# Kernel tuning notes

Hardware: AMD Instinct MI355X
Metric: run time of the kernel (lower is better)

The kernel has to match this reference:

```python
import jax, jax.numpy as jnp
import numpy as np

B, N, D = 8, 8192, 512
H, WIDTH = 8, 2048
DH = D // H
EPS = 1e-5


def _ln(x, g, b):
    m = jnp.mean(x, axis=-1, keepdims=True)
    v = jnp.mean(jnp.square(x - m), axis=-1, keepdims=True)
    return (x - m) * jax.lax.rsqrt(v + EPS) * g + b


def setup_inputs() -> dict:
    key = jax.random.key(0)
    ks = jax.random.split(key, 16)
    s = 0.02
    return {
        "x": jax.random.normal(ks[0], (B, N, D), dtype=jnp.float32),
        "mask": jnp.ones((B, N), dtype=jnp.float32),
        "Wq": jax.random.normal(ks[1], (D, D), dtype=jnp.float32) * s,
        "bq": jnp.zeros((D,), dtype=jnp.float32),
        "Wk": jax.random.normal(ks[2], (D, D), dtype=jnp.float32) * s,
        "bk": jnp.zeros((D,), dtype=jnp.float32),
        "Wv": jax.random.normal(ks[3], (D, D), dtype=jnp.float32) * s,
        "bv": jnp.zeros((D,), dtype=jnp.float32),
        "q_alpha": jax.random.normal(ks[4], (H, DH), dtype=jnp.float32),
        "k_beta": jax.random.normal(ks[5], (H, DH), dtype=jnp.float32),
        "Wo": jax.random.normal(ks[6], (D, D), dtype=jnp.float32) * s,
        "bo": jnp.zeros((D,), dtype=jnp.float32),
        "ln0_g": jnp.ones((D,), dtype=jnp.float32),
        "ln0_b": jnp.zeros((D,), dtype=jnp.float32),
        "ln1_g": jnp.ones((D,), dtype=jnp.float32),
        "ln1_b": jnp.zeros((D,), dtype=jnp.float32),
        "W1": jax.random.normal(ks[7], (WIDTH, D), dtype=jnp.float32) * s,
        "b1": jnp.zeros((WIDTH,), dtype=jnp.float32),
        "W2": jax.random.normal(ks[8], (D, WIDTH), dtype=jnp.float32) * s,
        "b2": jnp.zeros((D,), dtype=jnp.float32),
    }


def reference(x, mask, Wq, bq, Wk, bk, Wv, bv, q_alpha, k_beta, Wo, bo,
              ln0_g, ln0_b, ln1_g, ln1_b, W1, b1, W2, b2):
    scale = DH ** -0.5
    mask_ = mask[..., None]                       # [B,N,1]
    valid = (mask != 0)[..., None]                # [B,N,1] bool, broadcast over H

    residual = x
    xn = _ln(x, ln0_g, ln0_b) * mask_

    Q = (xn @ Wq.T + bq).reshape(B, N, H, DH)
    K = (xn @ Wk.T + bk).reshape(B, N, H, DH)
    V = (xn @ Wv.T + bv).reshape(B, N, H, DH)

    # stage 1: global query pooling
    alpha = jnp.einsum('bnhd,hd->bnh', Q, q_alpha) * scale
    alpha = jnp.where(valid, alpha, -jnp.inf)
    alpha = jax.nn.softmax(alpha, axis=1)         # softmax over N
    global_q = jnp.einsum('bnhd,bnh->bhd', Q, alpha)

    # stage 2: global value pooling
    P = K * global_q[:, None]                     # [B,N,H,DH]
    beta = jnp.einsum('bnhd,hd->bnh', P, k_beta) * scale
    beta = jnp.where(valid, beta, -jnp.inf)
    beta = jax.nn.softmax(beta, axis=1)
    global_v = jnp.einsum('bnhd,bnh->bhd', V, beta)

    out = (Q + global_v[:, None]).reshape(B, N, D)
    out = out @ Wo.T + bo
    x = residual + out

    residual = x
    xn = _ln(x, ln1_g, ln1_b)
    h = jax.nn.gelu(xn @ W1.T + b1, approximate=False)
    h = jax.nn.gelu(h @ W2.T + b2, approximate=False)
    x = residual + h
    x = x * mask_
    return x
```

## Files before the change

kernel.cpp:

```cpp
#include <hip/hip_runtime.h>
#include <hip/hip_bf16.h>
#include <hip/hip_fp8.h>
#include <math.h>

typedef short s8v __attribute__((ext_vector_type(8)));
typedef short s4v __attribute__((ext_vector_type(4)));
typedef __bf16 bf8v __attribute__((ext_vector_type(8)));
typedef float f4v __attribute__((ext_vector_type(4)));
typedef long l2v __attribute__((ext_vector_type(2)));

#define GLOBAL_AS __attribute__((address_space(1)))
#define LDS_AS __attribute__((address_space(3)))

static __device__ __forceinline__ float bf2f(ushort u) {
  return __builtin_bit_cast(float, (unsigned int)u << 16);
}
static __device__ __forceinline__ ushort f2bf(float f) {
  unsigned int u = __builtin_bit_cast(unsigned int, f);
  u += 0x7FFFu + ((u >> 16) & 1u);
  return (ushort)(u >> 16);
}
static __device__ __forceinline__ unsigned char f2fp8(float f) {
#if __has_builtin(__builtin_amdgcn_cvt_pk_fp8_f32)
  int p = __builtin_amdgcn_cvt_pk_fp8_f32(f, f, 0, false);
  return (unsigned char)(p & 0xFF);
#else
  __hip_fp8_e4m3 v(f);
  return (unsigned char)v.__x;
#endif
}
static __device__ __forceinline__ float gelu_f(float v) {
  float t = v * v;
  float u = v * (0.0356774081f * t + 0.7978845608f);
  float e = __expf(-2.0f * u);
  return v * __builtin_amdgcn_rcpf(1.0f + e);
}
static __device__ __forceinline__ float wave_max_f(float v) {
  #pragma unroll
  for (int o = 32; o >= 1; o >>= 1) v = fmaxf(v, __shfl_xor(v, o));
  return v;
}
static __device__ __forceinline__ float wave_sum_f(float v) {
  #pragma unroll
  for (int o = 32; o >= 1; o >>= 1) v += __shfl_xor(v, o);
  return v;
}
static __device__ __forceinline__ void gload16(const void* g, const void* l) {
  __builtin_amdgcn_global_load_lds(
      (const GLOBAL_AS unsigned int*)g,
      (LDS_AS unsigned int*)l, 16, 0, 0);
}

__global__ void cvt_f32_fp8il(const float* __restrict__ in,
                              unsigned char* __restrict__ out, int n, int kmask) {
  int i = (blockIdx.x * 256 + threadIdx.x) * 4;
  if (i >= n) return;
  float4 v = *(const float4*)(in + i);
  const int k = i & kmask;
  const int r = k & 63;
  const int qq = (r >> 3) & 3, h = (r >> 5) & 1, j = r & 7;
  const long o = (long)(i - r) + qq * 16 + h * 8 + j;
  uchar4 ob;
  ob.x = f2fp8(v.x * 8.f); ob.y = f2fp8(v.y * 8.f);
  ob.z = f2fp8(v.z * 8.f); ob.w = f2fp8(v.w * 8.f);
  *(uchar4*)(out + o) = ob;
}

__global__ void cvt_w1_fp8il(const float* __restrict__ in,
                             unsigned char* __restrict__ out) {
  int i = (blockIdx.x * 256 + threadIdx.x) * 4;
  const int ro = i >> 9;
  const int k4 = i & 511;
  const int g = ro >> 6, fr = ro & 63;
  const int L = fr & 15, nn = fr >> 4;
  const int sr = g * 64 + ((L >> 1) & 1) * 32 + (L >> 2) * 8 + (L & 1) * 4 + nn;
  float4 v = *(const float4*)(in + (long)sr * 512 + k4);
  const int r = k4 & 63;
  const int o = (k4 - r) + ((r >> 3) & 3) * 16 + (r >> 5) * 8 + (r & 7);
  uchar4 ob;
  ob.x = f2fp8(v.x * 8.f); ob.y = f2fp8(v.y * 8.f);
  ob.z = f2fp8(v.z * 8.f); ob.w = f2fp8(v.w * 8.f);
  *(uchar4*)(out + (long)ro * 512 + o) = ob;
}

__global__ void perm_b1(const float* __restrict__ b1, float* __restrict__ b1p) {
  const int p = blockIdx.x * 256 + threadIdx.x;
  const int g = p >> 6, r = p & 63;
  const int kc = ((r >> 3) & 1) * 32 + (r >> 4) * 8 + ((r >> 2) & 1) * 4 + (r & 3);
  b1p[p] = b1[g * 64 + kc];
}

__global__ __launch_bounds__(256) void transpose512(
    const float* __restrict__ in, float* __restrict__ out) {
  __shared__ float t[32][33];
  const int bx = blockIdx.x & 15, by = blockIdx.x >> 4;
  const int tx = threadIdx.x & 31, ty = threadIdx.x >> 5;
  #pragma unroll
  for (int i = 0; i < 4; ++i)
    t[ty + i * 8][tx] = in[(long)(by * 32 + ty + i * 8) * 512 + bx * 32 + tx];
  __syncthreads();
  #pragma unroll
  for (int i = 0; i < 4; ++i)
    out[(long)(bx * 32 + ty + i * 8) * 512 + by * 32 + tx] = t[tx][ty + i * 8];
}

__global__ __launch_bounds__(256) void wqo_kernel(
    const float* __restrict__ Wo, const float* __restrict__ Wq,
    ushort* __restrict__ WqoB)
{
  __shared__ float lO[64][33];
  __shared__ float lQ[32][65];
  const int t = threadIdx.x;
  const int bi = (blockIdx.x & 7) * 64, bj = (blockIdx.x >> 3) * 64;
  float acc[16] = {};
  for (int k0 = 0; k0 < 512; k0 += 32) {
    __syncthreads();
    {
      const int r = t >> 2, c = (t & 3) * 8;
      #pragma unroll
      for (int j = 0; j < 8; ++j) lO[r][c + j] = Wo[(long)(bi + r) * 512 + k0 + c + j];
      const int r2 = t >> 3, c2 = (t & 7) * 8;
      #pragma unroll
      for (int j = 0; j < 8; ++j) lQ[r2][c2 + j] = Wq[(long)(k0 + r2) * 512 + bj + c2 + j];
    }
    __syncthreads();
    const int j = t & 63, ig = t >> 6;
    for (int kk = 0; kk < 32; ++kk) {
      float q = lQ[kk][j];
      #pragma unroll
      for (int ii = 0; ii < 16; ++ii) acc[ii] += lO[ig * 16 + ii][kk] * q;
    }
  }
  const int j = t & 63, ig = t >> 6;
  #pragma unroll
  for (int ii = 0; ii < 16; ++ii)
    WqoB[(long)(bi + ig * 16 + ii) * 512 + bj + j] = f2bf(acc[ii]);
}

__global__ __launch_bounds__(256) void wa_kernel(
    const float* __restrict__ qa, const float* __restrict__ Wq,
    const float* __restrict__ bqv, ushort* __restrict__ waB, float* __restrict__ ca)
{
  __shared__ float ql[64];
  const int h = blockIdx.x;
  const int t = threadIdx.x;
  if (h >= 8) {
    waB[h * 512 + t] = 0; waB[h * 512 + 256 + t] = 0;
    if (t == 0) ca[h] = 0.f;
    return;
  }
  if (t < 64) ql[t] = qa[h * 64 + t];
  __syncthreads();
  #pragma unroll
  for (int half = 0; half < 2; ++half) {
    const int k = half * 256 + t;
    float s = 0;
    for (int dd = 0; dd < 64; ++dd) s += ql[dd] * Wq[(long)(h * 64 + dd) * 512 + k];
    waB[h * 512 + k] = f2bf(s);
  }
  if (t == 0) {
    float s = 0;
    for (int dd = 0; dd < 64; ++dd) s += ql[dd] * bqv[h * 64 + dd];
    ca[h] = s;
  }
}

__global__ __launch_bounds__(256) void ln0_alpha(
    const float* __restrict__ x, const float* __restrict__ gam,
    const float* __restrict__ bet, const float* __restrict__ mask,
    const ushort* __restrict__ waB, const float* __restrict__ ca,
    ushort* __restrict__ out, float* __restrict__ AL)
{
  __shared__ ushort wal[8 * 512];
  const int tid = threadIdx.x, lane = tid & 63, wv = tid >> 6;
  *(s8v*)(wal + tid * 8) = *(const s8v*)(waB + tid * 8);
  *(s8v*)(wal + 2048 + tid * 8) = *(const s8v*)(waB + 2048 + tid * 8);
  const float* gp = gam + lane * 8;
  const float* bp = bet + lane * 8;
  float4 g0 = *(const float4*)gp, g1 = *(const float4*)(gp + 4);
  float4 c0 = *(const float4*)bp, c1 = *(const float4*)(bp + 4);
  const float gg[8] = {g0.x, g0.y, g0.z, g0.w, g1.x, g1.y, g1.z, g1.w};
  const float cc[8] = {c0.x, c0.y, c0.z, c0.w, c1.x, c1.y, c1.z, c1.w};
  __syncthreads();
  const long row0 = (long)blockIdx.x * 16 + wv * 4;
  for (int rr = 0; rr < 4; ++rr) {
    const long row = row0 + rr;
    const float* xp = x + row * 512 + lane * 8;
    float4 a = *(const float4*)xp;
    float4 b = *(const float4*)(xp + 4);
    float s = a.x + a.y + a.z + a.w + b.x + b.y + b.z + b.w;
    float q = a.x*a.x + a.y*a.y + a.z*a.z + a.w*a.w
            + b.x*b.x + b.y*b.y + b.z*b.z + b.w*b.w;
    s = wave_sum_f(s); q = wave_sum_f(q);
    const float m = s * (1.f / 512.f);
    const float var = q * (1.f / 512.f) - m * m;
    const float r = rsqrtf(var + 1e-5f);
    const float mk = mask[row];
    const float xin[8] = {a.x, a.y, a.z, a.w, b.x, b.y, b.z, b.w};
    float of[8];
    s8v o;
    #pragma unroll
    for (int j = 0; j < 8; ++j) {
      of[j] = ((xin[j] - m) * r * gg[j] + cc[j]) * mk;
      o[j] = (short)f2bf(of[j]);
    }
    *(s8v*)(out + row * 512 + lane * 8) = o;
    float dh[8];
    #pragma unroll
    for (int h = 0; h < 8; ++h) {
      s8v wa8 = *(const s8v*)(wal + h * 512 + lane * 8);
      float d = 0.f;
      #pragma unroll
      for (int j = 0; j < 8; ++j) d += of[j] * bf2f((ushort)wa8[j]);
      dh[h] = wave_sum_f(d);
    }
    if (lane == 0) {
      const int bb = (int)(row >> 13);
      const int n = (int)(row & 8191);
      #pragma unroll
      for (int h = 0; h < 8; ++h) {
        float lg = (dh[h] + ca[h]) * 0.125f;
        if (mk == 0.f) lg = -1e30f;
        AL[((long)((bb << 3) + h) << 13) + n] = lg;
      }
    }
  }
}

__global__ __launch_bounds__(256) void ln_rows_fp8il(
    const ushort* __restrict__ x, const float* __restrict__ gam,
    const float* __restrict__ bet, unsigned char* __restrict__ out)
{
  const int tid = threadIdx.x, lane = tid & 63, wv = tid >> 6;
  const long row = (long)blockIdx.x * 4 + wv;
  s8v v = *(const s8v*)(x + row * 512 + lane * 8);
  float xv[8];
  #pragma unroll
  for (int j = 0; j < 8; ++j) xv[j] = bf2f((ushort)v[j]);
  float s = 0.f, q = 0.f;
  #pragma unroll
  for (int j = 0; j < 8; ++j) { s += xv[j]; q += xv[j] * xv[j]; }
  s = wave_sum_f(s); q = wave_sum_f(q);
  float m = s * (1.f / 512.f);
  float var = q * (1.f / 512.f) - m * m;
  float r = rsqrtf(var + 1e-5f);
  const float* gp = gam + lane * 8;
  const float* bp = bet + lane * 8;
  float4 g0 = *(const float4*)gp, g1 = *(const float4*)(gp + 4);
  float4 c0 = *(const float4*)bp, c1 = *(const float4*)(bp + 4);
  float gg[8] = {g0.x, g0.y, g0.z, g0.w, g1.x, g1.y, g1.z, g1.w};
  float cc[8] = {c0.x, c0.y, c0.z, c0.w, c1.x, c1.y, c1.z, c1.w};
  unsigned long long pk = 0;
  #pragma unroll
  for (int j = 0; j < 8; ++j) {
    unsigned char b8 = f2fp8((xv[j] - m) * r * gg[j] + cc[j]);
    pk |= (unsigned long long)b8 << (8 * j);
  }
  *(unsigned long long*)(out + row * 512 + (lane >> 3) * 64
                         + (lane & 3) * 16 + ((lane >> 2) & 1) * 8) = pk;
}

template<int BS, int CS>
__global__ __launch_bounds__(256) void logits_k(
    const ushort* __restrict__ XN, const ushort* __restrict__ Wl,
    const float* __restrict__ cvec, const float* __restrict__ mask,
    float* __restrict__ outL)
{
  __shared__ ushort lw[16 * 512];
  __shared__ __align__(16) ushort lx[64 * 512];
  const int tid = threadIdx.x, lane = tid & 63, wv = tid >> 6;
  const long r0 = (long)blockIdx.x * 64;
  const int b = (int)(r0 >> 13);
  #pragma unroll
  for (int i = 0; i < 16; ++i) {
    const int U = i * 256 + tid;
    const int r = U >> 6, u1 = U & 63;
    const int us = u1 ^ (r & 7);
    gload16(XN + (r0 + r) * 512 + us * 8, lx + (long)U * 8);
  }
  #pragma unroll
  for (int i = 0; i < 4; ++i) {
    const int u = tid + i * 256;
    const int h2 = u >> 6, uu = u & 63;
    s8v v = *(const s8v*)(Wl + (long)b * BS + h2 * 512 + uu * 8);
    *(s8v*)(lw + h2 * 512 + (uu ^ (h2 & 7)) * 8) = v;
  }
  __syncthreads();
  const int h = lane & 15, q = lane >> 4;
  const int rloc = wv * 16 + (lane & 15);
  const ushort* axp = lx + rloc * 512;
  f4v acc = {};
  #pragma unroll
  for (int t = 0; t < 16; ++t) {
    bf8v a = *(const bf8v*)(axp + (((t * 4 + q) ^ (rloc & 7))) * 8);
    bf8v bb = *(const bf8v*)(lw + h * 512 + (((t * 4 + q) ^ (h & 7))) * 8);
    acc = __builtin_amdgcn_mfma_f32_16x16x32_bf16(a, bb, acc, 0, 0, 0);
  }
  const float cv = cvec[b * CS + h];
  const long rw = r0 + wv * 16;
  #pragma unroll
  for (int j = 0; j < 4; ++j) {
    const long n = rw + q * 4 + j;
    float v = (acc[j] + cv) * 0.125f;
    if (mask[n] == 0.f) v = -1e30f;
    if (h < 8) outL[((long)((b << 3) + h) << 13) + (n & 8191)] = v;
  }
}

__global__ __launch_bounds__(1024) void softmax_rows(float* __restrict__ L)
{
  __shared__ float red[16];
  __shared__ float bc;
  const int tid = threadIdx.x, lane = tid & 63, wv = tid >> 6;
  float* p = L + ((long)blockIdx.x << 13) + tid * 8;
  float4 v0 = *(float4*)p;
  float4 v1 = *(float4*)(p + 4);
  float m = fmaxf(fmaxf(fmaxf(v0.x, v0.y), fmaxf(v0.z, v0.w)),
                  fmaxf(fmaxf(v1.x, v1.y), fmaxf(v1.z, v1.w)));
  m = wave_max_f(m);
  if (lane == 0) red[wv] = m;
  __syncthreads();
  if (tid < 64) {
    float t = (lane < 16) ? red[lane] : -INFINITY;
    t = wave_max_f(t);
    if (lane == 0) bc = t;
  }
  __syncthreads();
  const float gm = bc;
  v0.x = __expf(v0.x - gm); v0.y = __expf(v0.y - gm);
  v0.z = __expf(v0.z - gm); v0.w = __expf(v0.w - gm);
  v1.x = __expf(v1.x - gm); v1.y = __expf(v1.y - gm);
  v1.z = __expf(v1.z - gm); v1.w = __expf(v1.w - gm);
  float s = v0.x + v0.y + v0.z + v0.w + v1.x + v1.y + v1.z + v1.w;
  s = wave_sum_f(s);
  __syncthreads();
  if (lane == 0) red[wv] = s;
  __syncthreads();
  if (tid < 64) {
    float t = (lane < 16) ? red[lane] : 0.f;
    t = wave_sum_f(t);
    if (lane == 0) bc = t;
  }
  __syncthreads();
  const float inv = 1.0f / bc;
  v0.x *= inv; v0.y *= inv; v0.z *= inv; v0.w *= inv;
  v1.x *= inv; v1.y *= inv; v1.z *= inv; v1.w *= inv;
  *(float4*)p = v0;
  *(float4*)(p + 4) = v1;
}

__global__ __launch_bounds__(256) void pool_w(
    const ushort* __restrict__ XN, const float* __restrict__ wbuf,
    float* __restrict__ part)
{
  __shared__ float wlds[128][8];
  __shared__ float cmb[4][512];
  const int tid = threadIdx.x;
  const int b = blockIdx.x >> 6, ch = blockIdx.x & 63;
  const long g0 = ((long)b << 13) + ch * 128;
  if (tid < 128) {
    #pragma unroll
    for (int h = 0; h < 8; ++h)
      wlds[tid][h] = wbuf[(((long)(b * 8 + h)) << 13) + ch * 128 + tid];
  }
  __syncthreads();
  const int rg = tid >> 6, c8 = (tid & 63) * 8;
  f4v acc[8][2] = {};
  for (int it = 0; it < 32; ++it) {
    const int r = it * 4 + rg;
    s8v xv = *(const s8v*)(XN + (g0 + r) * 512 + c8);
    float xf[8];
    #pragma unroll
    for (int j = 0; j < 8; ++j) xf[j] = bf2f((ushort)xv[j]);
    #pragma unroll
    for (int h = 0; h < 8; ++h) {
      const float w = wlds[r][h];
      #pragma unroll
      for (int j = 0; j < 8; ++j) acc[h][j >> 2][j & 3] += w * xf[j];
    }
  }
  #pragma unroll
  for (int h = 0; h < 8; ++h) {
    __syncthreads();
    #pragma unroll
    for (int j = 0; j < 8; ++j) cmb[rg][c8 + j] = acc[h][j >> 2][j & 3];
    __syncthreads();
    const int col = tid * 2;
    float s0 = cmb[0][col] + cmb[1][col] + cmb[2][col] + cmb[3][col];
    float s1 = cmb[0][col + 1] + cmb[1][col + 1] + cmb[2][col + 1] + cmb[3][col + 1];
    *(float2*)(part + (((long)blockIdx.x * 8 + h) << 9) + col) = make_float2(s0, s1);
  }
}

__global__ __launch_bounds__(256) void combine_prep1(
    const float* __restrict__ part, const float* __restrict__ WqT,
    const float* __restrict__ bqv, const float* __restrict__ kbv,
    const float* __restrict__ Wk, const float* __restrict__ bkv,
    ushort* __restrict__ wbB, float* __restrict__ cbs)
{
  __shared__ float pxl[512];
  __shared__ float gkb[64];
  const int bh = blockIdx.x, b = bh >> 3, h = bh & 7;
  const int tid = threadIdx.x;
  {
    const int col = tid * 2;
    float s0 = 0.f, s1 = 0.f;
    for (int ch = 0; ch < 64; ++ch) {
      const float* p = part + (((long)((b * 64 + ch) * 8 + h)) << 9) + col;
      s0 += p[0]; s1 += p[1];
    }
    pxl[col] = s0; pxl[col + 1] = s1;
  }
  __syncthreads();
  if (tid < 64) {
    const int d = tid;
    float acc = bqv[h * 64 + d];
    for (int c = 0; c < 512; ++c) acc += pxl[c] * WqT[(long)c * 512 + h * 64 + d];
    gkb[d] = acc * kbv[h * 64 + d];
  }
  __syncthreads();
  if (tid < 64) {
    const int d = tid;
    float s[8] = {};
    for (int dd = 0; dd < 64; ++dd) {
      const float g = gkb[dd];
      const float* wr = Wk + (long)(h * 64 + dd) * 512 + d;
      #pragma unroll
      for (int ki = 0; ki < 8; ++ki) s[ki] += g * wr[ki * 64];
    }
    #pragma unroll
    for (int ki = 0; ki < 8; ++ki)
      wbB[(long)(b * 16 + h) * 512 + d + ki * 64] = f2bf(s[ki]);
    if (d == 0) {
      float t = 0.f;
      for (int dd = 0; dd < 64; ++dd) t += gkb[dd] * bkv[h * 64 + dd];
      cbs[b * 16 + h] = t;
    }
    if (h == 0) {
      #pragma unroll
      for (int hp = 8; hp < 16; ++hp)
        for (int k = d; k < 512; k += 64) wbB[(long)(b * 16 + hp) * 512 + k] = 0;
      if (d < 8) cbs[b * 16 + 8 + d] = 0.f;
    }
  }
}

__global__ __launch_bounds__(256) void combine_prep2(
    const float* __restrict__ part, const float* __restrict__ WvT,
    const float* __restrict__ bvv, const float* __restrict__ bqv,
    float* __restrict__ gvb)
{
  __shared__ float pxl[512];
  const int bh = blockIdx.x, b = bh >> 3, h = bh & 7;
  const int tid = threadIdx.x;
  {
    const int col = tid * 2;
    float s0 = 0.f, s1 = 0.f;
    for (int ch = 0; ch < 64; ++ch) {
      const float* p = part + (((long)((b * 64 + ch) * 8 + h)) << 9) + col;
      s0 += p[0]; s1 += p[1];
    }
    pxl[col] = s0; pxl[col + 1] = s1;
  }
  __syncthreads();
  if (tid < 64) {
    const int d = tid;
    float acc = bvv[h * 64 + d] + bqv[h * 64 + d];
    for (int c = 0; c < 512; ++c) acc += pxl[c] * WvT[(long)c * 512 + h * 64 + d];
    gvb[b * 512 + h * 64 + d] = acc;
  }
}

__global__ __launch_bounds__(256) void bias_gv(
    const float* __restrict__ gv, const float* __restrict__ Wo,
    const float* __restrict__ bo, float* __restrict__ bo2) {
  const int b = blockIdx.x;
  const int n = blockIdx.y * 256 + threadIdx.x;
  const float* g = gv + b * 512;
  const float* w = Wo + (long)n * 512;
  float acc = 0.f;
  for (int d = 0; d < 512; d += 4) {
    float4 wv4 = *(const float4*)(w + d);
    acc += g[d] * wv4.x + g[d + 1] * wv4.y + g[d + 2] * wv4.z + g[d + 3] * wv4.w;
  }
  bo2[b * 512 + n] = bo[n] + acc;
}

#define MFMA_(d,a,b) d = __builtin_amdgcn_mfma_f32_16x16x32_bf16(a, b, d, 0, 0, 0)

template<int EPI, int LDA, int NN, int KK>
__global__ __launch_bounds__(512, 4) void gemmP(
    const ushort* __restrict__ A, const ushort* __restrict__ W,
    const float* __restrict__ bias, const void* __restrict__ resid,
    const float* __restrict__ mask, void* __restrict__ Out)
{
  constexpr int NBX = NN / 256;
  constexpr int NT = KK / 32;
  __shared__ __align__(16) ushort lds[3][12288];
  const int tid = threadIdx.x;
  const int lane = tid & 63;
  const int w = tid >> 6;
  const int wm = w >> 2, wn = w & 3;

  const int nwg = gridDim.x;
  const int cpx = nwg >> 3;
  const int wg = (blockIdx.x & 7) * cpx + (blockIdx.x >> 3);
  const int bx = wg % NBX, by = wg / NBX;
  const long bm = (long)by * 128;
  const int bn = bx * 256;

  const int scr = tid >> 2, sls = tid & 3;
  const int akU = ((sls ^ (scr & 3) ^ ((scr >> 2) & 3))) * 8;
  const ushort* asrc = A + (bm + scr) * (long)LDA + akU;
  const int rbe = (scr & 31) + ((scr >> 5) << 6);
  const ushort* besrc = W + (long)(bn + rbe) * KK + akU;
  const ushort* bosrc = W + (long)(bn + rbe + 32) * KK + akU;

#define STG(b_, Tt) { \
    gload16(asrc + (Tt) * 32, &lds[b_][tid * 8]); \
    gload16(besrc + (Tt) * 32, &lds[b_][4096 + tid * 8]); \
    gload16(bosrc + (Tt) * 32, &lds[b_][8192 + tid * 8]); }

  STG(0, 0);
  STG(1, 1);

  f4v acc[4][4] = {};

  const int L = lane & 15, q = lane >> 4;
  const int soff = (q ^ (lane & 3) ^ ((lane >> 2) & 3)) * 8;
  const int abase = (wm * 64 + L) * 32 + soff;
  const int bbase = 4096 + (wn * 32 + L) * 32 + soff;

  asm volatile("s_waitcnt vmcnt(3)" ::: "memory");
  asm volatile("s_barrier" ::: "memory");

  for (int T = 0; T < NT; ++T) {
    const ushort* Lp = &lds[T % 3][0];
    bf8v aR[4], bR[4];
    #pragma unroll
    for (int m = 0; m < 4; ++m) aR[m] = *(const bf8v*)(Lp + abase + m * 512);
    bR[0] = *(const bf8v*)(Lp + bbase);
    bR[1] = *(const bf8v*)(Lp + bbase + 512);
    bR[2] = *(const bf8v*)(Lp + bbase + 4096);
    bR[3] = *(const bf8v*)(Lp + bbase + 4096 + 512);
    if (T + 2 < NT) {
      STG((T + 2) % 3, T + 2);
      asm volatile("s_waitcnt vmcnt(3)" ::: "memory");
    } else {
      asm volatile("s_waitcnt vmcnt(0)" ::: "memory");
    }
    asm volatile("s_barrier" ::: "memory");
    __builtin_amdgcn_s_setprio(1);
    #pragma unroll
    for (int m = 0; m < 4; ++m)
      #pragma unroll
      for (int n = 0; n < 4; ++n)
        MFMA_(acc[m][n], aR[m], bR[n]);
    __builtin_amdgcn_s_setprio(0);
  }
#undef STG

  const int colb = bn + wn * 64 + L;
  const long rowb = bm + wm * 64 + q * 4;
  const float* biasp = bias + ((bm >> 13) << 9);
  #pragma unroll
  for (int m = 0; m < 4; ++m) {
    #pragma unroll
    for (int j = 0; j < 4; ++j) {
      const long row = rowb + m * 16 + j;
      #pragma unroll
      for (int n = 0; n < 4; ++n) {
        const int col = colb + n * 16;
        float v = acc[m][n][j] + biasp[col];
        const long idx = row * (long)NN + col;
        ((ushort*)Out)[idx] = f2bf(v + ((const float*)resid)[idx]);
      }
    }
  }
}

template<int EPI, int NN, int KK>
__global__ __launch_bounds__(512, 4) void gemmF8(
    const unsigned char* __restrict__ A, const unsigned char* __restrict__ W,
    const float* __restrict__ bias, const void* __restrict__ resid,
    const float* __restrict__ mask, void* __restrict__ Out)
{
  constexpr int NBX = NN / 256;
  constexpr int NT = KK / 64;
  __shared__ __align__(16) unsigned char lds8[3][24576];
  const int tid = threadIdx.x;
  const int lane = tid & 63;
  const int w = tid >> 6;
  const int wm = w >> 2, wn = w & 3;

  const int nwg = gridDim.x;
  const int cpx = nwg >> 3;
  const int wg = (blockIdx.x & 7) * cpx + (blockIdx.x >> 3);
  const int bx = wg % NBX, by = wg / NBX;
  const long bm = (long)by * 128;
  const int bn = bx * 256;

  const int srow = tid >> 2;
  const int sgu = (tid & 3) ^ ((srow >> 1) & 3);
  const unsigned char* asrc = A + (bm + srow) * (long)KK + sgu * 16;
  const unsigned char* b0src = W + (long)(bn + srow) * KK + sgu * 16;
  const unsigned char* b1src = W + (long)(bn + 128 + srow) * KK + sgu * 16;

#define STG8(bf_, Tt) { \
    gload16(asrc + (Tt) * 64, &lds8[bf_][tid * 16]); \
    gload16(b0src + (Tt) * 64, &lds8[bf_][8192 + tid * 16]); \
    gload16(b1src + (Tt) * 64, &lds8[bf_][16384 + tid * 16]); }

  STG8(0, 0);
  STG8(1, 1);

  f4v acc[4][4] = {};

  const int L = lane & 15, q = lane >> 4;
  const int ua = (q ^ ((L >> 1) & 3)) * 16;
  const int arow = (wm * 64 + L) * 64;
  const int brow = 8192 + (wn * 64 + L) * 64;

  asm volatile("s_waitcnt vmcnt(3)" ::: "memory");
  asm volatile("s_barrier" ::: "memory");

  for (int T = 0; T < NT; ++T) {
    const unsigned char* Lp = &lds8[T % 3][0];
    l2v aV[4], bV[4];
    #pragma unroll
    for (int m = 0; m < 4; ++m) aV[m] = *(const l2v*)(Lp + arow + m * 1024 + ua);
    #pragma unroll
    for (int n = 0; n < 4; ++n) bV[n] = *(const l2v*)(Lp + brow + n * 1024 + ua);
    if (T + 2 < NT) {
      STG8((T + 2) % 3, T + 2);
      asm volatile("s_waitcnt vmcnt(3)" ::: "memory");
    } else {
      asm volatile("s_waitcnt vmcnt(0)" ::: "memory");
    }
    asm volatile("s_barrier" ::: "memory");
    __builtin_amdgcn_s_setprio(1);
    #pragma unroll
    for (int m = 0; m < 4; ++m)
      #pragma unroll
      for (int n = 0; n < 4; ++n) {
        acc[m][n] = __builtin_amdgcn_mfma_f32_16x16x32_fp8_fp8(
            aV[m][0], bV[n][0], acc[m][n], 0, 0, 0);
        acc[m][n] = __builtin_amdgcn_mfma_f32_16x16x32_fp8_fp8(
            aV[m][1], bV[n][1], acc[m][n], 0, 0, 0);
      }
    __builtin_amdgcn_s_setprio(0);
  }
#undef STG8

  const long rowb = bm + wm * 64 + q * 4;
  const int gbase = bn + wn * 64;
  if constexpr (EPI == 7) {
    const float4 bp4 = *(const float4*)(bias + gbase + 4 * L);
    #pragma unroll
    for (int m = 0; m < 4; ++m) {
      #pragma unroll
      for (int j = 0; j < 4; ++j) {
        const long row = rowb + m * 16 + j;
        float e0 = gelu_f(acc[m][0][j] * 0.125f + bp4.x);
        float e1 = gelu_f(acc[m][1][j] * 0.125f + bp4.y);
        float e2 = gelu_f(acc[m][2][j] * 0.125f + bp4.z);
        float e3 = gelu_f(acc[m][3][j] * 0.125f + bp4.w);
        unsigned int pw;
#if __has_builtin(__builtin_amdgcn_cvt_pk_fp8_f32)
        int t0 = __builtin_amdgcn_cvt_pk_fp8_f32(e0, e1, 0, false);
        pw = (unsigned int)__builtin_amdgcn_cvt_pk_fp8_f32(e2, e3, t0, true);
#else
        pw = (unsigned int)f2fp8(e0) | ((unsigned int)f2fp8(e1) << 8)
           | ((unsigned int)f2fp8(e2) << 16) | ((unsigned int)f2fp8(e3) << 24);
#endif
        *(unsigned int*)((unsigned char*)Out + row * (long)NN + gbase + 4 * L) = pw;
      }
    }
  } else {
    #pragma unroll
    for (int m = 0; m < 4; ++m) {
      #pragma unroll
      for (int j = 0; j < 4; ++j) {
        const long row = rowb + m * 16 + j;
        const float mk = mask[row];
        #pragma unroll
        for (int n = 0; n < 4; ++n) {
          const int col = gbase + n * 16 + L;
          float v = acc[m][n][j] * 0.125f + bias[col];
          const long idx = row * (long)NN + col;
          ((float*)Out)[idx] =
              (bf2f(((const ushort*)resid)[idx]) + gelu_f(v)) * mk;
        }
      }
    }
  }
}

extern "C" void kernel_launch(void* const* d_in, const int* in_sizes, int n_in,
                              void* d_out, int out_size, void* d_ws, size_t ws_size,
                              hipStream_t stream) {
  const float* x    = (const float*)d_in[0];
  const float* mask = (const float*)d_in[1];
  const float* Wq   = (const float*)d_in[2];
  const float* bq   = (const float*)d_in[3];
  const float* Wk   = (const float*)d_in[4];
  const float* bk   = (const float*)d_in[5];
  const float* Wv   = (const float*)d_in[6];
  const float* bv   = (const float*)d_in[7];
  const float* qa   = (const float*)d_in[8];
  const float* kb   = (const float*)d_in[9];
  const float* Wo   = (const float*)d_in[10];
  const float* bo   = (const float*)d_in[11];
  const float* g0   = (const float*)d_in[12];
  const float* be0  = (const float*)d_in[13];
  const float* g1   = (const float*)d_in[14];
  const float* be1  = (const float*)d_in[15];
  const float* W1   = (const float*)d_in[16];
  const float* b1   = (const float*)d_in[17];
  const float* W2   = (const float*)d_in[18];
  const float* b2   = (const float*)d_in[19];
  float* out = (float*)d_out;

  const int M = 65536;
  char* ws = (char*)d_ws;
  const size_t MB = 1024 * 1024;
  ushort* XN  = (ushort*)(ws);
  ushort* X1  = (ushort*)(ws + 64 * MB);
  unsigned char* XN1F = (unsigned char*)(ws + 128 * MB);
  unsigned char* H1F  = (unsigned char*)(ws + 192 * MB);
  float*  AL  = (float*)(ws + 320 * MB);
  float*  BL  = (float*)(ws + 322 * MB);
  float*  PART= (float*)(ws + 324 * MB);
  char* base = ws + 448 * MB;
  unsigned char* W1F = (unsigned char*)(base);
  unsigned char* W2F = (unsigned char*)(base + 2 * MB);
  ushort* WqoB = (ushort*)(base + 4 * MB);
  float*  WqT  = (float*)(base + 4 * MB + 512 * 1024);
  float*  WvT  = (float*)(base + 5 * MB + 512 * 1024);
  ushort* waB  = (ushort*)(base + 6 * MB + 512 * 1024);
  ushort* wbB  = (ushort*)(base + 6 * MB + 528 * 1024);
  float*  ca   = (float*)(base + 6 * MB + 656 * 1024);
  float*  cbs  = (float*)(base + 6 * MB + 660 * 1024);
  float*  GVB  = (float*)(base + 6 * MB + 920 * 1024);
  float*  BO2  = (float*)(base + 6 * MB + 936 * 1024);
  float*  B1P  = (float*)(base + 6 * MB + 952 * 1024);

  cvt_w1_fp8il<<<1024, 256, 0, stream>>>(W1, W1F);
  perm_b1<<<8, 256, 0, stream>>>(b1, B1P);
  cvt_f32_fp8il<<<1024, 256, 0, stream>>>(W2, W2F, 1048576, 2047);
  wqo_kernel<<<64, 256, 0, stream>>>(Wo, Wq, WqoB);
  wa_kernel<<<16, 256, 0, stream>>>(qa, Wq, bq, waB, ca);
  transpose512<<<256, 256, 0, stream>>>(Wq, WqT);
  transpose512<<<256, 256, 0, stream>>>(Wv, WvT);

  ln0_alpha<<<M / 16, 256, 0, stream>>>(x, g0, be0, mask, waB, ca, XN, AL);

  softmax_rows<<<64, 1024, 0, stream>>>(AL);
  pool_w<<<512, 256, 0, stream>>>(XN, AL, PART);
  combine_prep1<<<64, 256, 0, stream>>>(PART, WqT, bq, kb, Wk, bk, wbB, cbs);

  logits_k<8192, 16><<<1024, 256, 0, stream>>>(XN, wbB, cbs, mask, BL);
  softmax_rows<<<64, 1024, 0, stream>>>(BL);
  pool_w<<<512, 256, 0, stream>>>(XN, BL, PART);
  combine_prep2<<<64, 256, 0, stream>>>(PART, WvT, bv, bq, GVB);
  bias_gv<<<dim3(8, 2), 256, 0, stream>>>(GVB, Wo, bo, BO2);

  gemmP<5, 512, 512, 512><<<2 * (M / 128), 512, 0, stream>>>(
      XN, WqoB, BO2, x, nullptr, X1);

  ln_rows_fp8il<<<M / 4, 256, 0, stream>>>(X1, g1, be1, XN1F);

  gemmF8<7, 2048, 512><<<8 * (M / 128), 512, 0, stream>>>(
      XN1F, W1F, B1P, nullptr, nullptr, H1F);
  gemmF8<8, 512, 2048><<<2 * (M / 128), 512, 0, stream>>>(
      H1F, W2F, b2, X1, mask, out);
}
```

Baseline: 585.6 us.

## Switch second FFN GEMM from fp8 to int8 MFMA with fixed scaling

Replaces the fp8 path for the W2 GEMM with int8: W2 is quantized to int8 with a 1024 scale, the GELU output of the W1 GEMM is written as int8 with a 32 scale, and gemmW2 uses the 16x16x64 i8 MFMA with int32 accumulation. The int8 MFMA processes twice the K per instruction, which halves the MFMA instruction count in the K=2048 GEMM. The cost is coarser quantization: fixed scales clamp large activations and weights and give uniform rather than logarithmic precision, which could hurt accuracy.

```diff
diff --git a/kernel.cpp b/kernel.cpp
--- a/kernel.cpp
+++ b/kernel.cpp
@@ -8,6 +8,7 @@
 typedef __bf16 bf8v __attribute__((ext_vector_type(8)));
 typedef float f4v __attribute__((ext_vector_type(4)));
 typedef long l2v __attribute__((ext_vector_type(2)));
+typedef int i4v __attribute__((ext_vector_type(4)));
 
 #define GLOBAL_AS __attribute__((address_space(1)))
 #define LDS_AS __attribute__((address_space(3)))
@@ -29,6 +30,10 @@
   return (unsigned char)v.__x;
 #endif
 }
+static __device__ __forceinline__ int f2i8(float v) {
+  v = fminf(127.f, fmaxf(-127.f, v));
+  return __float2int_rn(v);
+}
 static __device__ __forceinline__ float gelu_f(float v) {
   float t = v * v;
   float u = v * (0.0356774081f * t + 0.7978845608f);
@@ -51,8 +56,8 @@
       (LDS_AS unsigned int*)l, 16, 0, 0);
 }
 
-__global__ void cvt_f32_fp8il(const float* __restrict__ in,
-                              unsigned char* __restrict__ out, int n, int kmask) {
+__global__ void cvt_f32_i8il(const float* __restrict__ in,
+                             unsigned char* __restrict__ out, int n, int kmask) {
   int i = (blockIdx.x * 256 + threadIdx.x) * 4;
   if (i >= n) return;
   float4 v = *(const float4*)(in + i);
@@ -61,8 +66,10 @@
   const int qq = (r >> 3) & 3, h = (r >> 5) & 1, j = r & 7;
   const long o = (long)(i - r) + qq * 16 + h * 8 + j;
   uchar4 ob;
-  ob.x = f2fp8(v.x * 8.f); ob.y = f2fp8(v.y * 8.f);
-  ob.z = f2fp8(v.z * 8.f); ob.w = f2fp8(v.w * 8.f);
+  ob.x = (unsigned char)(f2i8(v.x * 1024.f) & 255);
+  ob.y = (unsigned char)(f2i8(v.y * 1024.f) & 255);
+  ob.z = (unsigned char)(f2i8(v.z * 1024.f) & 255);
+  ob.w = (unsigned char)(f2i8(v.w * 1024.f) & 255);
   *(uchar4*)(out + o) = ob;
 }
 
@@ -579,12 +586,11 @@
   }
 }
 
-template<int EPI, int NN, int KK>
-__global__ __launch_bounds__(512, 4) void gemmF8(
+__global__ __launch_bounds__(512, 4) void gemmW1(
     const unsigned char* __restrict__ A, const unsigned char* __restrict__ W,
-    const float* __restrict__ bias, const void* __restrict__ resid,
-    const float* __restrict__ mask, void* __restrict__ Out)
-{
+    const float* __restrict__ bias, unsigned char* __restrict__ Out)
+{
+  constexpr int NN = 2048, KK = 512;
   constexpr int NBX = NN / 256;
   constexpr int NT = KK / 64;
   __shared__ __align__(16) unsigned char lds8[3][24576];
@@ -654,43 +660,113 @@
 
   const long rowb = bm + wm * 64 + q * 4;
   const int gbase = bn + wn * 64;
-  if constexpr (EPI == 7) {
-    const float4 bp4 = *(const float4*)(bias + gbase + 4 * L);
+  const float4 bp4 = *(const float4*)(bias + gbase + 4 * L);
+  #pragma unroll
+  for (int m = 0; m < 4; ++m) {
+    #pragma unroll
+    for (int j = 0; j < 4; ++j) {
+      const long row = rowb + m * 16 + j;
+      float e0 = gelu_f(acc[m][0][j] * 0.125f + bp4.x);
+      float e1 = gelu_f(acc[m][1][j] * 0.125f + bp4.y);
+      float e2 = gelu_f(acc[m][2][j] * 0.125f + bp4.z);
+      float e3 = gelu_f(acc[m][3][j] * 0.125f + bp4.w);
+      unsigned int pw =
+          ((unsigned)f2i8(e0 * 32.f) & 255u)
+        | (((unsigned)f2i8(e1 * 32.f) & 255u) << 8)
+        | (((unsigned)f2i8(e2 * 32.f) & 255u) << 16)
+        | (((unsigned)f2i8(e3 * 32.f) & 255u) << 24);
+      *(unsigned int*)(Out + row * (long)NN + gbase + 4 * L) = pw;
+    }
+  }
+}
+
+__global__ __launch_bounds__(512, 4) void gemmW2(
+    const unsigned char* __restrict__ A, const unsigned char* __restrict__ W,
+    const float* __restrict__ bias, const ushort* __restrict__ resid,
+    const float* __restrict__ mask, float* __restrict__ Out)
+{
+  constexpr int NN = 512, KK = 2048;
+  constexpr int NBX = NN / 256;
+  constexpr int NT = KK / 64;
+  __shared__ __align__(16) unsigned char lds8[3][24576];
+  const int tid = threadIdx.x;
+  const int lane = tid & 63;
+  const int w = tid >> 6;
+  const int wm = w >> 2, wn = w & 3;
+
+  const int nwg = gridDim.x;
+  const int cpx = nwg >> 3;
+  const int wg = (blockIdx.x & 7) * cpx + (blockIdx.x >> 3);
+  const int bx = wg % NBX, by = wg / NBX;
+  const long bm = (long)by * 128;
+  const int bn = bx * 256;
+
+  const int srow = tid >> 2;
+  const int sgu = (tid & 3) ^ ((srow >> 1) & 3);
+  const unsigned char* asrc = A + (bm + srow) * (long)KK + sgu * 16;
+  const unsigned char* b0src = W + (long)(bn + srow) * KK + sgu * 16;
+  const unsigned char* b1src = W + (long)(bn + 128 + srow) * KK + sgu * 16;
+
+#define STG8(bf_, Tt) { \
+    gload16(asrc + (Tt) * 64, &lds8[bf_][tid * 16]); \
+    gload16(b0src + (Tt) * 64, &lds8[bf_][8192 + tid * 16]); \
+    gload16(b1src + (Tt) * 64, &lds8[bf_][16384 + tid * 16]); }
+
+  STG8(0, 0);
+  STG8(1, 1);
+
+  i4v acc[4][4] = {};
+
+  const int L = lane & 15, q = lane >> 4;
+  const int ua = (q ^ ((L >> 1) & 3)) * 16;
+  const int arow = (wm * 64 + L) * 64;
+  const int brow = 8192 + (wn * 64 + L) * 64;
+
+  asm volatile("s_waitcnt vmcnt(3)" ::: "memory");
+  asm volatile("s_barrier" ::: "memory");
+
+  for (int T = 0; T < NT; ++T) {
+    const unsigned char* Lp = &lds8[T % 3][0];
+    l2v aV[4], bV[4];
+    #pragma unroll
+    for (int m = 0; m < 4; ++m) aV[m] = *(const l2v*)(Lp + arow + m * 1024 + ua);
+    #pragma unroll
+    for (int n = 0; n < 4; ++n) bV[n] = *(const l2v*)(Lp + brow + n * 1024 + ua);
+    if (T + 2 < NT) {
+      STG8((T + 2) % 3, T + 2);
+      asm volatile("s_waitcnt vmcnt(3)" ::: "memory");
+    } else {
+      asm volatile("s_waitcnt vmcnt(0)" ::: "memory");
+    }
+    asm volatile("s_barrier" ::: "memory");
+    __builtin_amdgcn_s_setprio(1);
     #pragma unroll
     for (int m = 0; m < 4; ++m) {
-      #pragma unroll
-      for (int j = 0; j < 4; ++j) {
-        const long row = rowb + m * 16 + j;
-        float e0 = gelu_f(acc[m][0][j] * 0.125f + bp4.x);
-        float e1 = gelu_f(acc[m][1][j] * 0.125f + bp4.y);
-        float e2 = gelu_f(acc[m][2][j] * 0.125f + bp4.z);
-        float e3 = gelu_f(acc[m][3][j] * 0.125f + bp4.w);
-        unsigned int pw;
-#if __has_builtin(__builtin_amdgcn_cvt_pk_fp8_f32)
-        int t0 = __builtin_amdgcn_cvt_pk_fp8_f32(e0, e1, 0, false);
-        pw = (unsigned int)__builtin_amdgcn_cvt_pk_fp8_f32(e2, e3, t0, true);
-#else
-        pw = (unsigned int)f2fp8(e0) | ((unsigned int)f2fp8(e1) << 8)
-           | ((unsigned int)f2fp8(e2) << 16) | ((unsigned int)f2fp8(e3) << 24);
-#endif
-        *(unsigned int*)((unsigned char*)Out + row * (long)NN + gbase + 4 * L) = pw;
+      const i4v am = __builtin_bit_cast(i4v, aV[m]);
+      #pragma unroll
+      for (int n = 0; n < 4; ++n) {
+        acc[m][n] = __builtin_amdgcn_mfma_i32_16x16x64_i8(
+            am, __builtin_bit_cast(i4v, bV[n]), acc[m][n], 0, 0, 0);
       }
     }
-  } else {
-    #pragma unroll
-    for (int m = 0; m < 4; ++m) {
-      #pragma unroll
-      for (int j = 0; j < 4; ++j) {
-        const long row = rowb + m * 16 + j;
-        const float mk = mask[row];
-        #pragma unroll
-        for (int n = 0; n < 4; ++n) {
-          const int col = gbase + n * 16 + L;
-          float v = acc[m][n][j] * 0.125f + bias[col];
-          const long idx = row * (long)NN + col;
-          ((float*)Out)[idx] =
-              (bf2f(((const ushort*)resid)[idx]) + gelu_f(v)) * mk;
-        }
+    __builtin_amdgcn_s_setprio(0);
+  }
+#undef STG8
+
+  const long rowb = bm + wm * 64 + q * 4;
+  const int gbase = bn + wn * 64;
+  #pragma unroll
+  for (int m = 0; m < 4; ++m) {
+    #pragma unroll
+    for (int j = 0; j < 4; ++j) {
+      const long row = rowb + m * 16 + j;
+      const float mk = mask[row];
+      #pragma unroll
+      for (int n = 0; n < 4; ++n) {
+        const int col = gbase + n * 16 + L;
+        float v = (float)acc[m][n][j] * (1.f / 32768.f) + bias[col];
+        const long idx = row * (long)NN + col;
+        Out[idx] = (bf2f(resid[idx]) + gelu_f(v)) * mk;
       }
     }
   }
@@ -747,7 +823,7 @@
 
   cvt_w1_fp8il<<<1024, 256, 0, stream>>>(W1, W1F);
   perm_b1<<<8, 256, 0, stream>>>(b1, B1P);
-  cvt_f32_fp8il<<<1024, 256, 0, stream>>>(W2, W2F, 1048576, 2047);
+  cvt_f32_i8il<<<1024, 256, 0, stream>>>(W2, W2F, 1048576, 2047);
   wqo_kernel<<<64, 256, 0, stream>>>(Wo, Wq, WqoB);
   wa_kernel<<<16, 256, 0, stream>>>(qa, Wq, bq, waB, ca);
   transpose512<<<256, 256, 0, stream>>>(Wq, WqT);
@@ -770,8 +846,6 @@
 
   ln_rows_fp8il<<<M / 4, 256, 0, stream>>>(X1, g1, be1, XN1F);
 
-  gemmF8<7, 2048, 512><<<8 * (M / 128), 512, 0, stream>>>(
-      XN1F, W1F, B1P, nullptr, nullptr, H1F);
-  gemmF8<8, 512, 2048><<<2 * (M / 128), 512, 0, stream>>>(
-      H1F, W2F, b2, X1, mask, out);
-}
+  gemmW1<<<8 * (M / 128), 512, 0, stream>>>(XN1F, W1F, B1P, H1F);
+  gemmW2<<<2 * (M / 128), 512, 0, stream>>>(H1F, W2F, b2, X1, mask, out);
+}
```

Measured after the change: 576.5 us. Within noise of the previous version (-1.6%).
